# Optimization experiments

Measured on AMD Instinct MI355X. Metric: run time of the kernel, lower is better.

The kernel has to match this reference:

```python
import jax, jax.numpy as jnp
import numpy as np

H = 4096          # hidden_size
HS = 64           # head_size
NH = H // HS      # num_heads = 64
TM = 64           # TIME_MIX_EXTRA_DIM (hidden_size == 4096)
TD = 128          # TIME_DECAY_EXTRA_DIM (hidden_size == 4096)
EPS = 1e-5


def _ln(v, w, b):
    mu = v.mean(-1, keepdims=True)
    var = v.var(-1, keepdims=True)
    return (v - mu) / jnp.sqrt(var + EPS) * w + b


def setup_inputs() -> dict:
    key = jax.random.key(0)
    ks = jax.random.split(key, 20)
    def n(i, shape, s=0.02):
        return jax.random.normal(ks[i], shape, dtype=jnp.float32) * s
    return {
        "x": n(0, (1, 1, H), 1.0),
        "state1": n(1, (1, 1, H), 1.0),
        "state2": n(2, (NH, HS, HS), 1.0),
        "ln1_w": jnp.ones((H,), jnp.float32),
        "ln1_b": jnp.zeros((H,), jnp.float32),
        "time_maa_x": n(3, (1, 1, H), 0.1),
        "time_maa": n(4, (5, 1, H), 0.1),       # stacked [w,k,v,r,g] mixes
        "maa_w1": n(5, (H, 5 * TM)),
        "maa_w2": n(6, (5, TM, H)),
        "time_decay": n(7, (NH, HS, 1), 0.5),
        "time_first": n(8, (NH, HS, 1), 0.5),
        "decay_w1": n(9, (H, TD)),
        "decay_w2": n(10, (TD, H)),
        "Wr": n(11, (H, H)),
        "Wk": n(12, (H, H)),
        "Wv": n(13, (H, H)),
        "Wg": n(14, (H, H)),
        "Wo": n(15, (H, H)),
        "lnx_w": jnp.ones((H,), jnp.float32),
        "lnx_b": jnp.zeros((H,), jnp.float32),
    }


def reference(x, state1, state2, ln1_w, ln1_b, time_maa_x, time_maa,
              maa_w1, maa_w2, time_decay, time_first, decay_w1, decay_w2,
              Wr, Wk, Wv, Wg, Wo, lnx_w, lnx_b):
    last_x = x
    xl = _ln(x, ln1_w, ln1_b)                         # [1,1,H]
    sx = state1 - xl                                  # token-shift delta
    xxx = xl + sx * time_maa_x                        # [1,1,H]
    xxx = jnp.tanh(xxx @ maa_w1).reshape(5, 1, TM)    # LoRA down, 5 mixes
    xxx = jnp.einsum('fot,fth->foh', xxx, maa_w2)     # LoRA up -> [5,1,H]
    xxx = xl + sx * (xxx + time_maa)                  # [5,1,H]
    mw, mk, mv, mr, mg = xxx[0], xxx[1], xxx[2], xxx[3], xxx[4]  # each [1,H]

    r = (mr @ Wr.T).reshape(NH, 1, HS)
    k = (mk @ Wk.T).reshape(NH, HS, 1)
    v = (mv @ Wv.T).reshape(NH, 1, HS)
    g = jax.nn.silu(mg @ Wg.T)                        # [1,H]

    # data-dependent decay (LoRA): exp(-exp(clip(w)))
    td = (jnp.tanh(mw @ decay_w1) @ decay_w2).reshape(NH, HS, 1) + time_decay
    td = jnp.exp(-jnp.exp(jnp.clip(td, -9.72, 2.27)))

    kv = k @ v                                        # [NH,HS,HS] outer product
    wkv = kv * time_first + state2                    # bonus + state
    out_h = (r @ wkv).reshape(NH, HS)                 # per-head readout
    state2_out = kv + state2 * td                     # state recurrence

    # InstanceNorm2d over head_size per head (no affine), then elementwise affine
    mu = out_h.mean(-1, keepdims=True)
    var = out_h.var(-1, keepdims=True)
    o = ((out_h - mu) / jnp.sqrt(var + EPS)).reshape(1, 1, H)
    o = o * lnx_w + lnx_b
    o = (o * g) @ Wo.T
    return (last_x + o, xl, state2_out)
```

## Files before the change

### kernel.cpp

```cpp
#include <hip/hip_runtime.h>
#include <hip/hip_bf16.h>


#define HDIM 4096

#define WS_XL    0
#define WS_SX    4096
#define WS_MV    8192
#define WS_PART  28672
#define WS_R     28672
#define WS_TD    45056
#define WS_DPART 49152
#define WS_OG    65536
#define WS_FLAG  69632

typedef unsigned short bfraw;

__device__ __forceinline__ float bf2f(bfraw u) {
    union { unsigned int u; float f; } v; v.u = ((unsigned int)u) << 16; return v.f;
}
__device__ __forceinline__ bfraw f2bf(float f) {
    union { float f; unsigned int u; } v; v.f = f;
    unsigned int u = v.u;
    unsigned int r = (u + 0x7fffu + ((u >> 16) & 1u)) >> 16;
    return (bfraw)r;
}
__device__ __forceinline__ float ldin(const void* p, long long i, bool isbf) {
    return isbf ? bf2f(((const bfraw*)p)[i]) : ((const float*)p)[i];
}
__device__ __forceinline__ void stout(void* p, long long i, float v, bool isbf) {
    if (isbf) ((bfraw*)p)[i] = f2bf(v); else ((float*)p)[i] = v;
}
__device__ __forceinline__ float waveReduce(float v) {
    for (int m = 32; m; m >>= 1) v += __shfl_xor(v, m);
    return v;
}

__device__ __forceinline__ void issue8(const bfraw* __restrict__ wr, int lane,
                                       uint4 buf[8]) {
    #pragma unroll
    for (int it = 0; it < 8; ++it)
        buf[it] = *(const uint4*)(wr + it * 512 + lane * 8);
}
__device__ __forceinline__ float consume8(const uint4 buf[8],
                                          const float* __restrict__ mLds, int lane) {
    float acc = 0.f;
    #pragma unroll
    for (int it = 0; it < 8; ++it) {
        int base = it * 512 + lane * 8;
        float4 m0 = *(const float4*)(mLds + base);
        float4 m1 = *(const float4*)(mLds + base + 4);
        uint4 w4 = buf[it];
        acc += bf2f((bfraw)(w4.x & 0xffff)) * m0.x + bf2f((bfraw)(w4.x >> 16)) * m0.y;
        acc += bf2f((bfraw)(w4.y & 0xffff)) * m0.z + bf2f((bfraw)(w4.y >> 16)) * m0.w;
        acc += bf2f((bfraw)(w4.z & 0xffff)) * m1.x + bf2f((bfraw)(w4.z >> 16)) * m1.y;
        acc += bf2f((bfraw)(w4.w & 0xffff)) * m1.z + bf2f((bfraw)(w4.w >> 16)) * m1.w;
    }
    return acc;
}
__device__ __forceinline__ float dot_row_f32(const float* __restrict__ wr,
                                             const float* __restrict__ mLds, int lane) {
    float acc = 0.f;
    #pragma unroll
    for (int h = 0; h < 2; ++h) {
        float4 av[8];
        #pragma unroll
        for (int it = 0; it < 8; ++it)
            av[it] = *(const float4*)(wr + h * 2048 + it * 256 + lane * 4);
        #pragma unroll
        for (int it = 0; it < 8; ++it) {
            int base = h * 2048 + it * 256 + lane * 4;
            float4 m0 = *(const float4*)(mLds + base);
            float4 a = av[it];
            acc += a.x * m0.x + a.y * m0.y + a.z * m0.z + a.w * m0.w;
        }
    }
    return acc;
}

__global__ __launch_bounds__(256)
void kA_ln_k2a(const void* __restrict__ x, const void* __restrict__ st1,
               const void* __restrict__ lnw, const void* __restrict__ lnb,
               const void* __restrict__ tmx, const void* __restrict__ w1,
               void* __restrict__ dout, float* __restrict__ ws) {
    int tid = threadIdx.x, b = blockIdx.x;
    int wid = tid >> 6, lane = tid & 63;
    bool isbf;
    {
        bfraw u = ((const bfraw*)x)[lane];
        int e = (u >> 7) & 0xFF;
        unsigned long long ball = __ballot(e >= 96 && e <= 144);
        isbf = __popcll(ball) >= 56;
    }
    if (b == 0 && tid == 0) ws[WS_FLAG] = isbf ? 1.0f : 0.0f;

    __shared__ float red[8];
    __shared__ float lx[64];
    float xv[16]; float s1 = 0.f, s2 = 0.f;
    for (int k = 0; k < 16; ++k) {
        float v = ldin(x, tid + k * 256, isbf);
        xv[k] = v; s1 += v; s2 += v * v;
    }
    s1 = waveReduce(s1); s2 = waveReduce(s2);
    if (lane == 0) { red[wid] = s1; red[4 + wid] = s2; }
    __syncthreads();
    float t1 = red[0] + red[1] + red[2] + red[3];
    float t2 = red[4] + red[5] + red[6] + red[7];
    float mu = t1 * (1.0f / HDIM);
    float var = fmaxf(t2 * (1.0f / HDIM) - mu * mu, 0.0f);
    float rstd = rsqrtf(var + 1e-5f);
    for (int k = 0; k < 16; ++k) {
        int i = tid + k * 256;
        if ((i >> 6) == b) {
            float xl = (xv[k] - mu) * rstd * ldin(lnw, i, isbf) + ldin(lnb, i, isbf);
            float sx = ldin(st1, i, isbf) - xl;
            float xxx = xl + sx * ldin(tmx, i, isbf);
            stout(dout, 4096 + i, xl, isbf);
            ws[WS_XL + i] = xl;
            ws[WS_SX + i] = sx;
            lx[i & 63] = xxx;
        }
    }
    __syncthreads();
    for (int c = tid; c < 320; c += 256) {
        float acc = 0.f;
        long long base = (long long)b * 64 * 320 + c;
        #pragma unroll 8
        for (int j = 0; j < 64; ++j)
            acc += lx[j] * ldin(w1, base + (long long)j * 320, isbf);
        ws[WS_PART + b * 320 + c] = acc;
    }
}

__global__ __launch_bounds__(256)
void kB_up_k3a(const void* __restrict__ w2, const void* __restrict__ tm,
               const void* __restrict__ dw1, float* __restrict__ ws) {
    bool isbf = ws[WS_FLAG] != 0.0f;
    int tid = threadIdx.x, b = blockIdx.x;
    __shared__ float zl[64];
    __shared__ float mwl[32];
    if (b < 80) {
        int f = b >> 4, hb = (b & 15) << 8;
        if (tid < 64) {
            float s = 0.f;
            #pragma unroll 8
            for (int p = 0; p < 64; ++p) s += ws[WS_PART + p * 320 + f * 64 + tid];
            zl[tid] = tanhf(s);
        }
        __syncthreads();
        int h = hb + tid;
        float acc = 0.f;
        long long base = (long long)f * 64 * HDIM + h;
        #pragma unroll 8
        for (int t = 0; t < 64; ++t)
            acc += zl[t] * ldin(w2, base + (long long)t * HDIM, isbf);
        float mval = ws[WS_XL + h] + ws[WS_SX + h] * (acc + ldin(tm, (long long)f * HDIM + h, isbf));
        ws[WS_MV + f * HDIM + h] = mval;
    } else {
        int d = b - 80;
        if (tid < 64) {
            float s = 0.f;
            #pragma unroll 8
            for (int p = 0; p < 64; ++p) s += ws[WS_PART + p * 320 + tid];
            zl[tid] = tanhf(s);
        }
        __syncthreads();
        if (tid < 32) {
            int h = d * 32 + tid;
            float acc = 0.f;
            #pragma unroll 8
            for (int t = 0; t < 64; ++t)
                acc += zl[t] * ldin(w2, (long long)t * HDIM + h, isbf);
            mwl[tid] = ws[WS_XL + h] + ws[WS_SX + h] * (acc + ldin(tm, h, isbf));
        }
        __syncthreads();
        if (tid < 128) {
            float acc = 0.f;
            long long base = (long long)d * 32 * 128 + tid;
            #pragma unroll 8
            for (int j = 0; j < 32; ++j)
                acc += mwl[j] * ldin(dw1, base + (long long)j * 128, isbf);
            ws[WS_DPART + d * 128 + tid] = acc;
        }
    }
}

__global__ __launch_bounds__(256)
void kC_k3b_k4(const void* __restrict__ dw2, const void* __restrict__ tdec,
               const void* __restrict__ Wr, const void* __restrict__ Wk,
               const void* __restrict__ Wv, const void* __restrict__ Wg,
               float* __restrict__ ws) {
    bool isbf = ws[WS_FLAG] != 0.0f;
    int tid = threadIdx.x;
    __shared__ __align__(16) float lm[HDIM];
    if (blockIdx.x < 32) {
        int bb = blockIdx.x;
        if (tid < 128) {
            float s = 0.f;
            #pragma unroll 8
            for (int p = 0; p < 128; ++p) s += ws[WS_DPART + p * 128 + tid];
            lm[tid] = tanhf(s);
        }
        __syncthreads();
        if (tid < 128) {
            int i = bb * 128 + tid;
            float acc = 0.f;
            #pragma unroll 8
            for (int t = 0; t < 128; ++t)
                acc += lm[t] * ldin(dw2, (long long)t * HDIM + i, isbf);
            float tv = acc + ldin(tdec, i, isbf);
            tv = fminf(fmaxf(tv, -9.72f), 2.27f);
            ws[WS_TD + i] = expf(-expf(tv));
        }
        return;
    }
    int k4b = blockIdx.x - 32;
    int wid = tid >> 6, lane = tid & 63;
    int mat = k4b >> 8;
    int bb = k4b & 255;
    const void* W; const float* msrc;
    if (mat == 0)      { W = Wr; msrc = ws + WS_MV + 3 * HDIM; }
    else if (mat == 1) { W = Wk; msrc = ws + WS_MV + 1 * HDIM; }
    else if (mat == 2) { W = Wv; msrc = ws + WS_MV + 2 * HDIM; }
    else               { W = Wg; msrc = ws + WS_MV + 4 * HDIM; }
    float* y = ws + WS_R + mat * HDIM;
    for (int i = tid * 4; i < HDIM; i += 1024)
        *(float4*)(lm + i) = *(const float4*)(msrc + i);
    __syncthreads();
    int r0 = bb * 16 + wid * 4;
    float acc0, acc1, acc2, acc3;
    if (isbf) {
        const bfraw* w0 = (const bfraw*)W + (long long)r0 * HDIM;
        uint4 A[8], B[8];
        issue8(w0, lane, A);
        issue8(w0 + HDIM, lane, B);
        __builtin_amdgcn_sched_barrier(0);
        acc0 = consume8(A, lm, lane);
        issue8(w0 + 2 * HDIM, lane, A);
        __builtin_amdgcn_sched_barrier(0);
        acc1 = consume8(B, lm, lane);
        issue8(w0 + 3 * HDIM, lane, B);
        __builtin_amdgcn_sched_barrier(0);
        acc2 = consume8(A, lm, lane);
        acc3 = consume8(B, lm, lane);
    } else {
        const float* w0 = (const float*)W + (long long)r0 * HDIM;
        acc0 = dot_row_f32(w0, lm, lane);
        acc1 = dot_row_f32(w0 + HDIM, lm, lane);
        acc2 = dot_row_f32(w0 + 2 * HDIM, lm, lane);
        acc3 = dot_row_f32(w0 + 3 * HDIM, lm, lane);
    }
    acc0 = waveReduce(acc0); acc1 = waveReduce(acc1);
    acc2 = waveReduce(acc2); acc3 = waveReduce(acc3);
    if (lane == 0) {
        if (mat == 3) {
            acc0 = acc0 / (1.0f + expf(-acc0));
            acc1 = acc1 / (1.0f + expf(-acc1));
            acc2 = acc2 / (1.0f + expf(-acc2));
            acc3 = acc3 / (1.0f + expf(-acc3));
        }
        y[r0] = acc0; y[r0 + 1] = acc1; y[r0 + 2] = acc2; y[r0 + 3] = acc3;
    }
}

__global__ __launch_bounds__(64)
void kD_heads(const void* __restrict__ state2, const void* __restrict__ tfirst,
              const void* __restrict__ lnxw, const void* __restrict__ lnxb,
              void* __restrict__ dout, float* __restrict__ ws) {
    bool isbf = ws[WS_FLAG] != 0.0f;
    int h = blockIdx.x, j = threadIdx.x;
    int gi = h * 64 + j;
    float rj = ws[WS_R + gi], kj = ws[WS_R + HDIM + gi];
    float vj = ws[WS_R + 2 * HDIM + gi], gj = ws[WS_R + 3 * HDIM + gi];
    float tdj = ws[WS_TD + gi];
    float tfj = ldin(tfirst, gi, isbf);
    __shared__ float lr[64], lk[64], ltd[64];
    lr[j] = rj; lk[j] = kj; ltd[j] = tdj;
    float c = waveReduce(rj * kj * tfj);
    __syncthreads();
    float acc = 0.f;
    long long sbase = (long long)h * 4096 + j;
    #pragma unroll 8
    for (int i = 0; i < 64; ++i) {
        float s = ldin(state2, sbase + i * 64, isbf);
        acc += lr[i] * s;
        stout(dout, 8192 + sbase + i * 64, lk[i] * vj + s * ltd[i], isbf);
    }
    float oh = vj * c + acc;
    float s1 = waveReduce(oh);
    float s2 = waveReduce(oh * oh);
    float mu = s1 * (1.0f / 64.0f);
    float var = fmaxf(s2 * (1.0f / 64.0f) - mu * mu, 0.0f);
    float rstd = rsqrtf(var + 1e-5f);
    float o = (oh - mu) * rstd * ldin(lnxw, gi, isbf) + ldin(lnxb, gi, isbf);
    ws[WS_OG + gi] = o * gj;
}

__global__ __launch_bounds__(256)
void kE_out(const void* __restrict__ Wo, const void* __restrict__ x,
            void* __restrict__ dout, float* __restrict__ ws) {
    bool isbf = ws[WS_FLAG] != 0.0f;
    int tid = threadIdx.x;
    int wid = tid >> 6, lane = tid & 63;
    __shared__ __align__(16) float lm[HDIM];
    for (int i = tid * 4; i < HDIM; i += 1024)
        *(float4*)(lm + i) = *(const float4*)(ws + WS_OG + i);
    __syncthreads();
    int r0 = blockIdx.x * 8 + wid * 2;
    float acc0, acc1;
    if (isbf) {
        const bfraw* w0 = (const bfraw*)Wo + (long long)r0 * HDIM;
        uint4 A[8], B[8];
        issue8(w0, lane, A);
        issue8(w0 + HDIM, lane, B);
        __builtin_amdgcn_sched_barrier(0);
        acc0 = consume8(A, lm, lane);
        acc1 = consume8(B, lm, lane);
    } else {
        const float* w0 = (const float*)Wo + (long long)r0 * HDIM;
        acc0 = dot_row_f32(w0, lm, lane);
        acc1 = dot_row_f32(w0 + HDIM, lm, lane);
    }
    acc0 = waveReduce(acc0); acc1 = waveReduce(acc1);
    if (lane == 0) {
        stout(dout, r0,     ldin(x, r0, isbf)     + acc0, isbf);
        stout(dout, r0 + 1, ldin(x, r0 + 1, isbf) + acc1, isbf);
    }
}

extern "C" void kernel_launch(void* const* d_in, const int* in_sizes, int n_in,
                              void* d_out, int out_size, void* d_ws, size_t ws_size,
                              hipStream_t stream) {
    const void* x      = d_in[0];
    const void* st1    = d_in[1];
    const void* st2    = d_in[2];
    const void* ln1w   = d_in[3];
    const void* ln1b   = d_in[4];
    const void* tmx    = d_in[5];
    const void* tmaa   = d_in[6];
    const void* maw1   = d_in[7];
    const void* maw2   = d_in[8];
    const void* tdec   = d_in[9];
    const void* tfirst = d_in[10];
    const void* dw1    = d_in[11];
    const void* dw2    = d_in[12];
    const void* Wr     = d_in[13];
    const void* Wk     = d_in[14];
    const void* Wv     = d_in[15];
    const void* Wg     = d_in[16];
    const void* Wo     = d_in[17];
    const void* lnxw   = d_in[18];
    const void* lnxb   = d_in[19];

    float* ws = (float*)d_ws;

    kA_ln_k2a<<<64, 256, 0, stream>>>(x, st1, ln1w, ln1b, tmx, maw1, d_out, ws);
    kB_up_k3a<<<208, 256, 0, stream>>>(maw2, tmaa, dw1, ws);
    kC_k3b_k4<<<1056, 256, 0, stream>>>(dw2, tdec, Wr, Wk, Wv, Wg, ws);
    kD_heads<<<64, 64, 0, stream>>>(st2, tfirst, lnxw, lnxb, d_out, ws);
    kE_out<<<512, 256, 0, stream>>>(Wo, x, d_out, ws);
}
```

Baseline: 392.2 us.

## Fuse LayerNorm, LoRA down and up into one kernel; merge decay LoRA

The LayerNorm, time-mix LoRA down-projection and up-projection now run in a single 80-block kernel. Each block recomputes the full LayerNorm and the down-projection for its mix, so the partial-sum workspace round trip and one kernel launch go away. The decay LoRA (dw1 then dw2) moves into 4 blocks of the big projection kernel, and the old 32-block decay stage is removed. In exchange, the maa_w1 down-projection is computed redundantly 16 times per mix (about 5 MB of reads), the decay path runs on only 4 blocks with long serial loops, and those blocks may finish after the GEMV blocks.

```diff
diff --git a/kernel.cpp b/kernel.cpp
--- a/kernel.cpp
+++ b/kernel.cpp
@@ -3,16 +3,13 @@
 
 
 #define HDIM 4096
-
-#define WS_XL    0
-#define WS_SX    4096
-#define WS_MV    8192
-#define WS_PART  28672
-#define WS_R     28672
-#define WS_TD    45056
-#define WS_DPART 49152
-#define WS_OG    65536
-#define WS_FLAG  69632
+#define KC_BLOCKS 1028
+
+#define WS_MV    0
+#define WS_TD    20480
+#define WS_R     24576
+#define WS_OG    40960
+#define WS_FLAG  45056
 
 typedef unsigned short bfraw;
 
@@ -79,23 +76,27 @@
 }
 
 __global__ __launch_bounds__(256)
-void kA_ln_k2a(const void* __restrict__ x, const void* __restrict__ st1,
-               const void* __restrict__ lnw, const void* __restrict__ lnb,
-               const void* __restrict__ tmx, const void* __restrict__ w1,
-               void* __restrict__ dout, float* __restrict__ ws) {
-    int tid = threadIdx.x, b = blockIdx.x;
+void kS_fused(const void* __restrict__ x, const void* __restrict__ st1,
+              const void* __restrict__ lnw, const void* __restrict__ lnb,
+              const void* __restrict__ tmx, const void* __restrict__ tm,
+              const void* __restrict__ w1, const void* __restrict__ w2,
+              void* __restrict__ dout, float* __restrict__ ws) {
+    int tid = threadIdx.x, u = blockIdx.x;
+    int f = u >> 4, hs = u & 15;
     int wid = tid >> 6, lane = tid & 63;
     bool isbf;
     {
-        bfraw u = ((const bfraw*)x)[lane];
-        int e = (u >> 7) & 0xFF;
+        bfraw uu = ((const bfraw*)x)[lane];
+        int e = (uu >> 7) & 0xFF;
         unsigned long long ball = __ballot(e >= 96 && e <= 144);
         isbf = __popcll(ball) >= 56;
     }
-    if (b == 0 && tid == 0) ws[WS_FLAG] = isbf ? 1.0f : 0.0f;
+    if (u == 0 && tid == 0) ws[WS_FLAG] = isbf ? 1.0f : 0.0f;
 
     __shared__ float red[8];
-    __shared__ float lx[64];
+    __shared__ __align__(16) float xxxL[HDIM];
+    __shared__ float zpart[4][64];
+    __shared__ float zlL[64];
     float xv[16]; float s1 = 0.f, s2 = 0.f;
     for (int k = 0; k < 16; ++k) {
         float v = ldin(x, tid + k * 256, isbf);
@@ -109,115 +110,84 @@
     float mu = t1 * (1.0f / HDIM);
     float var = fmaxf(t2 * (1.0f / HDIM) - mu * mu, 0.0f);
     float rstd = rsqrtf(var + 1e-5f);
+    float xl_m = 0.f, sx_m = 0.f;
     for (int k = 0; k < 16; ++k) {
         int i = tid + k * 256;
-        if ((i >> 6) == b) {
-            float xl = (xv[k] - mu) * rstd * ldin(lnw, i, isbf) + ldin(lnb, i, isbf);
-            float sx = ldin(st1, i, isbf) - xl;
-            float xxx = xl + sx * ldin(tmx, i, isbf);
-            stout(dout, 4096 + i, xl, isbf);
-            ws[WS_XL + i] = xl;
-            ws[WS_SX + i] = sx;
-            lx[i & 63] = xxx;
-        }
-    }
-    __syncthreads();
-    for (int c = tid; c < 320; c += 256) {
+        float xl = (xv[k] - mu) * rstd * ldin(lnw, i, isbf) + ldin(lnb, i, isbf);
+        float sx = ldin(st1, i, isbf) - xl;
+        xxxL[i] = xl + sx * ldin(tmx, i, isbf);
+        if (k == hs) {
+            xl_m = xl; sx_m = sx;
+            if (f == 0) stout(dout, 4096 + i, xl, isbf);
+        }
+    }
+    __syncthreads();
+    {
+        int t = lane;
         float acc = 0.f;
-        long long base = (long long)b * 64 * 320 + c;
+        long long coff = (long long)f * 64 + t;
+        int j0 = wid * 1024;
         #pragma unroll 8
-        for (int j = 0; j < 64; ++j)
-            acc += lx[j] * ldin(w1, base + (long long)j * 320, isbf);
-        ws[WS_PART + b * 320 + c] = acc;
-    }
+        for (int j = j0; j < j0 + 1024; ++j)
+            acc += xxxL[j] * ldin(w1, (long long)j * 320 + coff, isbf);
+        zpart[wid][t] = acc;
+    }
+    __syncthreads();
+    if (tid < 64)
+        zlL[tid] = tanhf(zpart[0][tid] + zpart[1][tid] + zpart[2][tid] + zpart[3][tid]);
+    __syncthreads();
+    int h = (hs << 8) + tid;
+    float acc = 0.f;
+    long long base = (long long)f * 64 * HDIM + h;
+    #pragma unroll 8
+    for (int t = 0; t < 64; ++t)
+        acc += zlL[t] * ldin(w2, base + (long long)t * HDIM, isbf);
+    ws[WS_MV + f * HDIM + h] = xl_m + sx_m * (acc + ldin(tm, (long long)f * HDIM + h, isbf));
 }
 
 __global__ __launch_bounds__(256)
-void kB_up_k3a(const void* __restrict__ w2, const void* __restrict__ tm,
-               const void* __restrict__ dw1, float* __restrict__ ws) {
+void kC_big(const void* __restrict__ dw1, const void* __restrict__ dw2,
+            const void* __restrict__ tdec,
+            const void* __restrict__ Wr, const void* __restrict__ Wk,
+            const void* __restrict__ Wv, const void* __restrict__ Wg,
+            float* __restrict__ ws) {
     bool isbf = ws[WS_FLAG] != 0.0f;
-    int tid = threadIdx.x, b = blockIdx.x;
-    __shared__ float zl[64];
-    __shared__ float mwl[32];
-    if (b < 80) {
-        int f = b >> 4, hb = (b & 15) << 8;
-        if (tid < 64) {
-            float s = 0.f;
+    int tid = threadIdx.x, bid = blockIdx.x;
+    int wid = tid >> 6, lane = tid & 63;
+    __shared__ __align__(16) float lm[HDIM];
+    __shared__ float zr2[2][128];
+    __shared__ float dzS[128];
+
+    if (bid < 4) {
+        for (int i = tid * 4; i < HDIM; i += 1024)
+            *(float4*)(lm + i) = *(const float4*)(ws + WS_MV + i);
+        __syncthreads();
+        {
+            int t = tid & 127, hf = tid >> 7;
+            float acc = 0.f;
+            int j0 = hf * 2048;
             #pragma unroll 8
-            for (int p = 0; p < 64; ++p) s += ws[WS_PART + p * 320 + f * 64 + tid];
-            zl[tid] = tanhf(s);
+            for (int j = j0; j < j0 + 2048; ++j)
+                acc += lm[j] * ldin(dw1, (long long)j * 128 + t, isbf);
+            zr2[hf][t] = acc;
         }
         __syncthreads();
-        int h = hb + tid;
-        float acc = 0.f;
-        long long base = (long long)f * 64 * HDIM + h;
-        #pragma unroll 8
-        for (int t = 0; t < 64; ++t)
-            acc += zl[t] * ldin(w2, base + (long long)t * HDIM, isbf);
-        float mval = ws[WS_XL + h] + ws[WS_SX + h] * (acc + ldin(tm, (long long)f * HDIM + h, isbf));
-        ws[WS_MV + f * HDIM + h] = mval;
-    } else {
-        int d = b - 80;
-        if (tid < 64) {
-            float s = 0.f;
-            #pragma unroll 8
-            for (int p = 0; p < 64; ++p) s += ws[WS_PART + p * 320 + tid];
-            zl[tid] = tanhf(s);
-        }
+        if (tid < 128) dzS[tid] = tanhf(zr2[0][tid] + zr2[1][tid]);
         __syncthreads();
-        if (tid < 32) {
-            int h = d * 32 + tid;
-            float acc = 0.f;
-            #pragma unroll 8
-            for (int t = 0; t < 64; ++t)
-                acc += zl[t] * ldin(w2, (long long)t * HDIM + h, isbf);
-            mwl[tid] = ws[WS_XL + h] + ws[WS_SX + h] * (acc + ldin(tm, h, isbf));
-        }
-        __syncthreads();
-        if (tid < 128) {
-            float acc = 0.f;
-            long long base = (long long)d * 32 * 128 + tid;
-            #pragma unroll 8
-            for (int j = 0; j < 32; ++j)
-                acc += mwl[j] * ldin(dw1, base + (long long)j * 128, isbf);
-            ws[WS_DPART + d * 128 + tid] = acc;
-        }
-    }
-}
-
-__global__ __launch_bounds__(256)
-void kC_k3b_k4(const void* __restrict__ dw2, const void* __restrict__ tdec,
-               const void* __restrict__ Wr, const void* __restrict__ Wk,
-               const void* __restrict__ Wv, const void* __restrict__ Wg,
-               float* __restrict__ ws) {
-    bool isbf = ws[WS_FLAG] != 0.0f;
-    int tid = threadIdx.x;
-    __shared__ __align__(16) float lm[HDIM];
-    if (blockIdx.x < 32) {
-        int bb = blockIdx.x;
-        if (tid < 128) {
-            float s = 0.f;
-            #pragma unroll 8
-            for (int p = 0; p < 128; ++p) s += ws[WS_DPART + p * 128 + tid];
-            lm[tid] = tanhf(s);
-        }
-        __syncthreads();
-        if (tid < 128) {
-            int i = bb * 128 + tid;
-            float acc = 0.f;
+        for (int k = 0; k < 4; ++k) {
+            int i = bid * 1024 + k * 256 + tid;
+            float a = 0.f;
             #pragma unroll 8
             for (int t = 0; t < 128; ++t)
-                acc += lm[t] * ldin(dw2, (long long)t * HDIM + i, isbf);
-            float tv = acc + ldin(tdec, i, isbf);
+                a += dzS[t] * ldin(dw2, (long long)t * HDIM + i, isbf);
+            float tv = a + ldin(tdec, i, isbf);
             tv = fminf(fmaxf(tv, -9.72f), 2.27f);
             ws[WS_TD + i] = expf(-expf(tv));
         }
         return;
     }
-    int k4b = blockIdx.x - 32;
-    int wid = tid >> 6, lane = tid & 63;
-    int mat = k4b >> 8;
-    int bb = k4b & 255;
+    int k4b = bid - 4;
+    int mat = k4b >> 8, bb = k4b & 255;
     const void* W; const float* msrc;
     if (mat == 0)      { W = Wr; msrc = ws + WS_MV + 3 * HDIM; }
     else if (mat == 1) { W = Wk; msrc = ws + WS_MV + 1 * HDIM; }
@@ -354,9 +324,10 @@
 
     float* ws = (float*)d_ws;
 
-    kA_ln_k2a<<<64, 256, 0, stream>>>(x, st1, ln1w, ln1b, tmx, maw1, d_out, ws);
-    kB_up_k3a<<<208, 256, 0, stream>>>(maw2, tmaa, dw1, ws);
-    kC_k3b_k4<<<1056, 256, 0, stream>>>(dw2, tdec, Wr, Wk, Wv, Wg, ws);
+    kS_fused<<<80, 256, 0, stream>>>(x, st1, ln1w, ln1b, tmx, tmaa,
+                                     maw1, maw2, d_out, ws);
+    kC_big<<<KC_BLOCKS, 256, 0, stream>>>(dw1, dw2, tdec,
+                                          Wr, Wk, Wv, Wg, ws);
     kD_heads<<<64, 64, 0, stream>>>(st2, tfirst, lnxw, lnxb, d_out, ws);
     kE_out<<<512, 256, 0, stream>>>(Wo, x, d_out, ws);
 }
```

Result: slower. 634.0 us (+61.7%).
